# Kernel optimization log

Measured on AMD Instinct MI355X. Metric: run time of the kernel, lower is better.

Reference implementation:

```python
import jax, jax.numpy as jnp
import numpy as np

N, E, D_IN, D_OUT, R = 50000, 800000, 128, 128, 8


def setup_inputs() -> dict:
    key = jax.random.key(0)
    ks = jax.random.split(key, 6)
    x = jax.random.normal(ks[0], (N, D_IN), dtype=jnp.float32)
    W_rel = jax.random.normal(ks[1], (R, D_IN, D_OUT), dtype=jnp.float32) * (1.0 / np.sqrt(D_IN))
    W_self_w = jax.random.normal(ks[2], (D_OUT, D_IN), dtype=jnp.float32) * (1.0 / np.sqrt(D_IN))
    W_self_b = jax.random.normal(ks[3], (D_OUT,), dtype=jnp.float32) * 0.01
    edge_index = jax.random.randint(ks[4], (2, E), 0, N, dtype=jnp.int32)
    edge_type = jax.random.randint(ks[5], (E,), 0, R, dtype=jnp.int32)
    return {"x": x, "W_rel": W_rel, "W_self_w": W_self_w, "W_self_b": W_self_b,
            "edge_index": edge_index, "edge_type": edge_type}


def reference(x, W_rel, W_self_w, W_self_b, edge_index, edge_type):
    n = x.shape[0]
    # self-loop linear (nn.Linear: y = x @ W.T + b)
    out = x @ W_self_w.T + W_self_b
    src = edge_index[0]
    dst = edge_index[1]
    # Per-relation transform of all nodes: h[r, n, :] = x[n] @ W_rel[r]
    # (mathematically identical to per-edge bmm(x[src], W_rel[rel]))
    h = jnp.einsum('nd,rdo->rno', x, W_rel)  # [R, N, D_OUT]
    msg = h[edge_type, src]                   # [E, D_OUT] gather
    agg = jax.ops.segment_sum(msg, dst, num_segments=n)  # scatter-add
    deg = jax.ops.segment_sum(jnp.ones_like(dst, dtype=x.dtype), dst, num_segments=n)
    deg = jnp.maximum(deg, 1.0)[:, None]
    out = jax.nn.relu(out + agg / deg)
    # dropout p=0.0 / eval mode -> identity
    return out
```

## Files before the change

kernel.cpp:

```cpp
#include <hip/hip_runtime.h>
#include <hip/hip_bf16.h>


#define D 128
#define RNUM 8
#define KREL (RNUM * D)
#define KTOT (KREL + D)
#define ZCH 64
#define ZNB 64
#define ZSP 72

#define BSHIFT 6
#define BRANGE 64
#define BCAP   2048
#define NBKT_MAX 784
#define CSTRIDE 16

typedef short short8 __attribute__((ext_vector_type(8)));
typedef float float4v __attribute__((ext_vector_type(4)));
typedef float float2v __attribute__((ext_vector_type(2)));

static __device__ __forceinline__ unsigned int f2b(float f) {
    unsigned int u = __float_as_uint(f);
    return (u + 0x7fffu + ((u >> 16) & 1u)) >> 16;
}
static __device__ __forceinline__ float b2f_lo(unsigned int u) {
    return __uint_as_float(u << 16);
}
static __device__ __forceinline__ float b2f_hi(unsigned int u) {
    return __uint_as_float(u & 0xffff0000u);
}

static __device__ __forceinline__ void gl_lds16(const void* g, void* l) {
    __builtin_amdgcn_global_load_lds(
        (const __attribute__((address_space(1))) unsigned int*)g,
        (__attribute__((address_space(3))) unsigned int*)l, 16, 0, 0);
}

__global__ void prep_kernel(const float* __restrict__ x,
                            const float* __restrict__ W_rel,
                            const float* __restrict__ W_self,
                            unsigned short* __restrict__ xb,
                            unsigned short* __restrict__ Wcol,
                            int* __restrict__ gcur,
                            int Nn, int xb_blocks, int wc_blocks, int gz) {
    if (blockIdx.x < (unsigned)xb_blocks) {
        int t = blockIdx.x * 256 + threadIdx.x;
        int n = t >> 5;
        int c = (t & 31) * 4;
        if (n >= Nn) return;
        float4 v = *(const float4*)(x + (size_t)n * D + c);
        unsigned int p0 = f2b(v.x) | (f2b(v.y) << 16);
        unsigned int p1 = f2b(v.z) | (f2b(v.w) << 16);
        *(uint2*)(xb + (size_t)n * D + c) = make_uint2(p0, p1);
    } else if (blockIdx.x < (unsigned)(xb_blocks + wc_blocks)) {
        int idx = (blockIdx.x - xb_blocks) * 256 + threadIdx.x;
        if (idx >= KTOT * D) return;
        int c = idx >> 7;
        int k = idx & 127;
        float v = (c < KREL)
            ? W_rel[(size_t)((c >> 7) * D + k) * D + (c & 127)]
            : W_self[(size_t)(c - KREL) * D + k];
        Wcol[idx] = (unsigned short)f2b(v);
    } else {
        int idx = (blockIdx.x - xb_blocks - wc_blocks) * 256 + threadIdx.x;
        if (idx < gz) gcur[idx] = 0;
    }
}

__global__ __launch_bounds__(256) void coarse_kernel(
        const int* __restrict__ ei, const int* __restrict__ et,
        int* __restrict__ gcur, int* __restrict__ data, int E, int nbkt) {
    __shared__ int cnt[NBKT_MAX];
    int t = threadIdx.x;
    for (int i = t; i < nbkt; i += 256) cnt[i] = 0;
    __syncthreads();

    int rec[8], rb[8], rk[8];
    int e0 = blockIdx.x * 2048;
#pragma unroll
    for (int j = 0; j < 8; ++j) {
        int e = e0 + j * 256 + t;
        bool ok = e < E;
        int s = ok ? ei[e] : 0;
        int d = ok ? ei[E + e] : 0;
        int r = ok ? et[e] : 0;
        int bkt = d >> BSHIFT;
        rec[j] = s | ((d & (BRANGE - 1)) << 16) | (r << 22);
        rb[j] = ok ? bkt : -1;
        rk[j] = ok ? atomicAdd(&cnt[bkt], 1) : 0;
    }
    __syncthreads();

    for (int i = t; i < nbkt; i += 256) {
        int c = cnt[i];
        if (c) cnt[i] = i * BCAP + atomicAdd(&gcur[i * CSTRIDE], c);
    }
    __syncthreads();

#pragma unroll
    for (int j = 0; j < 8; ++j) {
        if (rb[j] >= 0) {
            int pos = cnt[rb[j]] + rk[j];
            if (pos < (rb[j] + 1) * BCAP)
                data[pos] = rec[j];
        }
    }
}

__global__ __launch_bounds__(256) void fine_kernel(
        int* __restrict__ data, const int* __restrict__ gcur,
        int* __restrict__ offsets, int* __restrict__ deg, int Nn) {
    __shared__ int recs[BCAP];
    __shared__ int hist[BRANGE * RNUM];
    int b = blockIdx.x;
    int t = threadIdx.x;
    int gbase = b * BCAP;
    int cnt = gcur[b * CSTRIDE];
    if (cnt > BCAP) cnt = BCAP;

    for (int i = t; i < BRANGE * RNUM; i += 256) hist[i] = 0;
    __syncthreads();

    for (int i = t; i < cnt; i += 256) {
        int rec = data[gbase + i];
        recs[i] = rec;
        int n = (rec >> 16) & (BRANGE - 1);
        int r = (rec >> 22) & 7;
        atomicAdd(&hist[n * RNUM + r], 1);
    }
    __syncthreads();

    if (t < BRANGE) {
        int dsum = 0;
#pragma unroll
        for (int r = 0; r < RNUM; ++r) dsum += hist[t * RNUM + r];
        int pad = (dsum + 7) & ~7;
        int x = pad;
        for (int off = 1; off < 64; off <<= 1) {
            int y = __shfl_up(x, off);
            if (t >= off) x += y;
        }
        int nb = gbase + (x - pad);
        int n0 = b * BRANGE + t;
        if (n0 < Nn) { offsets[n0] = nb; deg[n0] = dsum; }
        for (int i = dsum; i < pad; ++i)
            data[nb + i] = (int)0xF0000000u;
        int q = nb;
#pragma unroll
        for (int r = 0; r < RNUM; ++r) { int c = hist[t * RNUM + r]; hist[t * RNUM + r] = q; q += c; }
    }
    __syncthreads();

    for (int i = t; i < cnt; i += 256) {
        int rec = recs[i];
        int n = (rec >> 16) & (BRANGE - 1);
        int r = (rec >> 22) & 7;
        int pos = atomicAdd(&hist[n * RNUM + r], 1);
        data[pos] = (rec & 0xFFFF) | (r << 28);
    }
}

__global__ __launch_bounds__(256) void zgemm_kernel(
        const unsigned short* __restrict__ xb,
        const unsigned short* __restrict__ Wcol,
        unsigned short* __restrict__ Z) {
    __shared__ unsigned short Ws[ZCH * 128];
    __shared__ unsigned short Zs[ZNB * ZSP];

    const int tid  = threadIdx.x;
    const int lane = tid & 63;
    const int w    = tid >> 6;
    const int l16  = lane & 15;
    const int q    = lane >> 4;
    const int c0   = blockIdx.x * ZCH;
    const int n0   = blockIdx.y * ZNB;
    const int n    = n0 + w * 16 + l16;

    short8 xq[4];
#pragma unroll
    for (int kw = 0; kw < 4; ++kw)
        xq[kw] = *(const short8*)(xb + (size_t)n * D + kw * 32 + q * 8);

#pragma unroll
    for (int i = 0; i < 4; ++i) {
        int s = i * 256 + w * 64 + lane;
        int c = s >> 4;
        int p = (s & 15) ^ (c & 15);
        gl_lds16(Wcol + (size_t)(c0 + c) * D + p * 8,
                 &Ws[(size_t)(i * 256 + w * 64) * 8]);
    }
    __syncthreads();

    float4v acc[4] = {};
#pragma unroll
    for (int cg = 0; cg < 4; ++cg) {
#pragma unroll
        for (int kw = 0; kw < 4; ++kw) {
            short8 a = *(const short8*)(
                &Ws[(((cg * 16 + l16) << 4) + ((kw * 4 + q) ^ l16)) * 8]);
            acc[cg] = __builtin_amdgcn_mfma_f32_16x16x32_bf16(
                a, xq[kw], acc[cg], 0, 0, 0);
        }
    }

#pragma unroll
    for (int cg = 0; cg < 4; ++cg) {
        unsigned int lo = f2b(acc[cg][0]) | (f2b(acc[cg][1]) << 16);
        unsigned int hi = f2b(acc[cg][2]) | (f2b(acc[cg][3]) << 16);
        *(uint2*)(&Zs[(w * 16 + l16) * ZSP + cg * 16 + q * 4]) = make_uint2(lo, hi);
    }
    __syncthreads();

    {
        int row = tid >> 2;
        int pc  = (tid & 3) * 8;
        short8 z0 = *(const short8*)(&Zs[row * ZSP + pc]);
        short8 z1 = *(const short8*)(&Zs[row * ZSP + pc + 32]);
        unsigned short* dst = Z + (size_t)(n0 + row) * KTOT + c0;
        *(short8*)(dst + pc)      = z0;
        *(short8*)(dst + pc + 32) = z1;
    }
}

__global__ __launch_bounds__(256) void gather_kernel(
        const unsigned short* __restrict__ Z,
        const int* __restrict__ offsets,
        const int* __restrict__ deg,
        const int* __restrict__ sorted,
        const float* __restrict__ bias,
        float* __restrict__ out,
        int Nn) {
    int node = blockIdx.x * 4 + (threadIdx.x >> 6);
    if (node >= Nn) return;
    int lane = threadIdx.x & 63;
    int laneoff = lane * 2;

    int b0 = __builtin_amdgcn_readfirstlane(offsets[node]);
    int dg = __builtin_amdgcn_readfirstlane(deg[node]);
    float inv = 1.0f / fmaxf((float)dg, 1.0f);
    int bulk = dg & ~7;
    int rem  = dg & 7;

    float2v racc = {0.0f, 0.0f};

    for (int e = b0; e < b0 + bulk; e += 8) {
        int pv[8];
#pragma unroll
        for (int j = 0; j < 8; ++j)
            pv[j] = __builtin_amdgcn_readfirstlane(sorted[e + j]);
        unsigned int u[8];
#pragma unroll
        for (int j = 0; j < 8; ++j) {
            int src = pv[j] & 0xFFFF;
            int rel = (((unsigned)pv[j]) >> 28) & 7;
            u[j] = *(const unsigned int*)(Z + (size_t)src * KTOT + rel * D + laneoff);
        }
#pragma unroll
        for (int j = 0; j < 8; ++j) {
            racc.x += b2f_lo(u[j]);
            racc.y += b2f_hi(u[j]);
        }
    }
    if (rem) {
        int e = b0 + bulk;
        int pv[8];
#pragma unroll
        for (int j = 0; j < 8; ++j)
            pv[j] = __builtin_amdgcn_readfirstlane(sorted[e + j]);
        unsigned int u[8];
#pragma unroll
        for (int j = 0; j < 8; ++j) {
            int src = pv[j] & 0xFFFF;
            int rel = (((unsigned)pv[j]) >> 28) & 7;
            u[j] = *(const unsigned int*)(Z + (size_t)src * KTOT + rel * D + laneoff);
        }
#pragma unroll
        for (int j = 0; j < 8; ++j) {
            if (j < rem) {
                racc.x += b2f_lo(u[j]);
                racc.y += b2f_hi(u[j]);
            }
        }
    }

    unsigned int zs = *(const unsigned int*)(Z + (size_t)node * KTOT + KREL + laneoff);
    float bx = bias[laneoff];
    float by = bias[laneoff + 1];
    float o0 = fmaxf(b2f_lo(zs) + bx + racc.x * inv, 0.0f);
    float o1 = fmaxf(b2f_hi(zs) + by + racc.y * inv, 0.0f);
    *(float2*)(out + (size_t)node * D + laneoff) = make_float2(o0, o1);
}

extern "C" void kernel_launch(void* const* d_in, const int* in_sizes, int n_in,
                              void* d_out, int out_size, void* d_ws, size_t ws_size,
                              hipStream_t stream) {
    const float* x      = (const float*)d_in[0];
    const float* W_rel  = (const float*)d_in[1];
    const float* W_self = (const float*)d_in[2];
    const float* W_bias = (const float*)d_in[3];
    const int*   ei     = (const int*)d_in[4];
    const int*   et     = (const int*)d_in[5];

    const int Nn = in_sizes[0] / D;
    const int E  = in_sizes[4] / 2;
    const int npad = ((Nn + ZNB - 1) / ZNB) * ZNB;
    const int nbkt = (Nn + BRANGE - 1) >> BSHIFT;
    const int gz   = nbkt * CSTRIDE;

    char* p = (char*)d_ws;
    auto take = [&](size_t bytes) { char* q = p; p += (bytes + 255) & ~(size_t)255; return q; };
    unsigned short* Z    = (unsigned short*)take((size_t)npad * KTOT * sizeof(unsigned short));
    unsigned short* xb   = (unsigned short*)take((size_t)npad * D * sizeof(unsigned short));
    unsigned short* Wcol = (unsigned short*)take((size_t)KTOT * D * sizeof(unsigned short));
    int* offsets = (int*)take((size_t)Nn * sizeof(int));
    int* deg     = (int*)take((size_t)Nn * sizeof(int));
    int* gcur    = (int*)take((size_t)gz * sizeof(int));
    int* data    = (int*)take((size_t)nbkt * BCAP * sizeof(int));

    const int xb_blocks = (Nn * 32 + 255) / 256;
    const int wc_blocks = (KTOT * D + 255) / 256;
    const int gz_blocks = (gz + 255) / 256;
    prep_kernel<<<xb_blocks + wc_blocks + gz_blocks, 256, 0, stream>>>(
        x, W_rel, W_self, xb, Wcol, gcur, Nn, xb_blocks, wc_blocks, gz);
    coarse_kernel<<<(E + 2047) / 2048, 256, 0, stream>>>(ei, et, gcur, data, E, nbkt);
    fine_kernel<<<nbkt, 256, 0, stream>>>(data, gcur, offsets, deg, Nn);
    dim3 zgrid(KTOT / ZCH, npad / ZNB);
    zgemm_kernel<<<zgrid, 256, 0, stream>>>(xb, Wcol, Z);
    gather_kernel<<<(Nn + 3) / 4, 256, 0, stream>>>(Z, offsets, deg, data, W_bias,
                                                    (float*)d_out, Nn);
}
```

Baseline: 199.3 us.

## Fuse prep with coarse bucketing and zgemm with fine sort; XCD-aware strip mapping

Merges the conversion/prep kernel with the coarse edge bucketing kernel, and the Z GEMM with the fine per-node sort, into single heterogeneous launches. The counter zeroing moves to a hipMemsetAsync. The GEMM blocks are remapped so each XCD handles contiguous node strips across all 18 column chunks, which should improve L2 reuse of xb. This cuts launch count and lets the independent stages overlap on the GPU. In exchange it raises shared memory per block to the larger of the two roles and adds branch divergence between block types.

```diff
diff --git a/kernel.cpp b/kernel.cpp
--- a/kernel.cpp
+++ b/kernel.cpp
@@ -37,13 +37,16 @@
         (__attribute__((address_space(3))) unsigned int*)l, 16, 0, 0);
 }
 
-__global__ void prep_kernel(const float* __restrict__ x,
-                            const float* __restrict__ W_rel,
-                            const float* __restrict__ W_self,
-                            unsigned short* __restrict__ xb,
-                            unsigned short* __restrict__ Wcol,
-                            int* __restrict__ gcur,
-                            int Nn, int xb_blocks, int wc_blocks, int gz) {
+__global__ __launch_bounds__(256) void prep_coarse_kernel(
+        const float* __restrict__ x,
+        const float* __restrict__ W_rel,
+        const float* __restrict__ W_self,
+        const int* __restrict__ ei, const int* __restrict__ et,
+        unsigned short* __restrict__ xb,
+        unsigned short* __restrict__ Wcol,
+        int* __restrict__ gcur, int* __restrict__ data,
+        int Nn, int E, int xb_blocks, int wc_blocks, int nbkt) {
+    __shared__ int cnt[NBKT_MAX];
     if (blockIdx.x < (unsigned)xb_blocks) {
         int t = blockIdx.x * 256 + threadIdx.x;
         int n = t >> 5;
@@ -63,163 +66,167 @@
             : W_self[(size_t)(c - KREL) * D + k];
         Wcol[idx] = (unsigned short)f2b(v);
     } else {
-        int idx = (blockIdx.x - xb_blocks - wc_blocks) * 256 + threadIdx.x;
-        if (idx < gz) gcur[idx] = 0;
+        int blk = blockIdx.x - xb_blocks - wc_blocks;
+        int t = threadIdx.x;
+        for (int i = t; i < nbkt; i += 256) cnt[i] = 0;
+        __syncthreads();
+
+        int rec[8], rb[8], rk[8];
+        int e0 = blk * 2048;
+#pragma unroll
+        for (int j = 0; j < 8; ++j) {
+            int e = e0 + j * 256 + t;
+            bool ok = e < E;
+            int s = ok ? ei[e] : 0;
+            int d = ok ? ei[E + e] : 0;
+            int r = ok ? et[e] : 0;
+            int bkt = d >> BSHIFT;
+            rec[j] = s | ((d & (BRANGE - 1)) << 16) | (r << 22);
+            rb[j] = ok ? bkt : -1;
+            rk[j] = ok ? atomicAdd(&cnt[bkt], 1) : 0;
+        }
+        __syncthreads();
+
+        for (int i = t; i < nbkt; i += 256) {
+            int c = cnt[i];
+            if (c) cnt[i] = i * BCAP + atomicAdd(&gcur[i * CSTRIDE], c);
+        }
+        __syncthreads();
+
+#pragma unroll
+        for (int j = 0; j < 8; ++j) {
+            if (rb[j] >= 0) {
+                int pos = cnt[rb[j]] + rk[j];
+                if (pos < (rb[j] + 1) * BCAP)
+                    data[pos] = rec[j];
+            }
+        }
     }
 }
 
-__global__ __launch_bounds__(256) void coarse_kernel(
-        const int* __restrict__ ei, const int* __restrict__ et,
-        int* __restrict__ gcur, int* __restrict__ data, int E, int nbkt) {
-    __shared__ int cnt[NBKT_MAX];
-    int t = threadIdx.x;
-    for (int i = t; i < nbkt; i += 256) cnt[i] = 0;
-    __syncthreads();
-
-    int rec[8], rb[8], rk[8];
-    int e0 = blockIdx.x * 2048;
-#pragma unroll
-    for (int j = 0; j < 8; ++j) {
-        int e = e0 + j * 256 + t;
-        bool ok = e < E;
-        int s = ok ? ei[e] : 0;
-        int d = ok ? ei[E + e] : 0;
-        int r = ok ? et[e] : 0;
-        int bkt = d >> BSHIFT;
-        rec[j] = s | ((d & (BRANGE - 1)) << 16) | (r << 22);
-        rb[j] = ok ? bkt : -1;
-        rk[j] = ok ? atomicAdd(&cnt[bkt], 1) : 0;
-    }
-    __syncthreads();
-
-    for (int i = t; i < nbkt; i += 256) {
-        int c = cnt[i];
-        if (c) cnt[i] = i * BCAP + atomicAdd(&gcur[i * CSTRIDE], c);
-    }
-    __syncthreads();
-
-#pragma unroll
-    for (int j = 0; j < 8; ++j) {
-        if (rb[j] >= 0) {
-            int pos = cnt[rb[j]] + rk[j];
-            if (pos < (rb[j] + 1) * BCAP)
-                data[pos] = rec[j];
-        }
-    }
-}
-
-__global__ __launch_bounds__(256) void fine_kernel(
-        int* __restrict__ data, const int* __restrict__ gcur,
-        int* __restrict__ offsets, int* __restrict__ deg, int Nn) {
-    __shared__ int recs[BCAP];
-    __shared__ int hist[BRANGE * RNUM];
-    int b = blockIdx.x;
-    int t = threadIdx.x;
-    int gbase = b * BCAP;
-    int cnt = gcur[b * CSTRIDE];
-    if (cnt > BCAP) cnt = BCAP;
-
-    for (int i = t; i < BRANGE * RNUM; i += 256) hist[i] = 0;
-    __syncthreads();
-
-    for (int i = t; i < cnt; i += 256) {
-        int rec = data[gbase + i];
-        recs[i] = rec;
-        int n = (rec >> 16) & (BRANGE - 1);
-        int r = (rec >> 22) & 7;
-        atomicAdd(&hist[n * RNUM + r], 1);
-    }
-    __syncthreads();
-
-    if (t < BRANGE) {
-        int dsum = 0;
-#pragma unroll
-        for (int r = 0; r < RNUM; ++r) dsum += hist[t * RNUM + r];
-        int pad = (dsum + 7) & ~7;
-        int x = pad;
-        for (int off = 1; off < 64; off <<= 1) {
-            int y = __shfl_up(x, off);
-            if (t >= off) x += y;
-        }
-        int nb = gbase + (x - pad);
-        int n0 = b * BRANGE + t;
-        if (n0 < Nn) { offsets[n0] = nb; deg[n0] = dsum; }
-        for (int i = dsum; i < pad; ++i)
-            data[nb + i] = (int)0xF0000000u;
-        int q = nb;
-#pragma unroll
-        for (int r = 0; r < RNUM; ++r) { int c = hist[t * RNUM + r]; hist[t * RNUM + r] = q; q += c; }
-    }
-    __syncthreads();
-
-    for (int i = t; i < cnt; i += 256) {
-        int rec = recs[i];
-        int n = (rec >> 16) & (BRANGE - 1);
-        int r = (rec >> 22) & 7;
-        int pos = atomicAdd(&hist[n * RNUM + r], 1);
-        data[pos] = (rec & 0xFFFF) | (r << 28);
-    }
-}
-
-__global__ __launch_bounds__(256) void zgemm_kernel(
+__global__ __launch_bounds__(256) void zgemm_fine_kernel(
         const unsigned short* __restrict__ xb,
         const unsigned short* __restrict__ Wcol,
-        unsigned short* __restrict__ Z) {
-    __shared__ unsigned short Ws[ZCH * 128];
-    __shared__ unsigned short Zs[ZNB * ZSP];
-
-    const int tid  = threadIdx.x;
-    const int lane = tid & 63;
-    const int w    = tid >> 6;
-    const int l16  = lane & 15;
-    const int q    = lane >> 4;
-    const int c0   = blockIdx.x * ZCH;
-    const int n0   = blockIdx.y * ZNB;
-    const int n    = n0 + w * 16 + l16;
-
-    short8 xq[4];
-#pragma unroll
-    for (int kw = 0; kw < 4; ++kw)
-        xq[kw] = *(const short8*)(xb + (size_t)n * D + kw * 32 + q * 8);
-
-#pragma unroll
-    for (int i = 0; i < 4; ++i) {
-        int s = i * 256 + w * 64 + lane;
-        int c = s >> 4;
-        int p = (s & 15) ^ (c & 15);
-        gl_lds16(Wcol + (size_t)(c0 + c) * D + p * 8,
-                 &Ws[(size_t)(i * 256 + w * 64) * 8]);
-    }
-    __syncthreads();
-
-    float4v acc[4] = {};
-#pragma unroll
-    for (int cg = 0; cg < 4; ++cg) {
-#pragma unroll
-        for (int kw = 0; kw < 4; ++kw) {
-            short8 a = *(const short8*)(
-                &Ws[(((cg * 16 + l16) << 4) + ((kw * 4 + q) ^ l16)) * 8]);
-            acc[cg] = __builtin_amdgcn_mfma_f32_16x16x32_bf16(
-                a, xq[kw], acc[cg], 0, 0, 0);
-        }
-    }
-
-#pragma unroll
-    for (int cg = 0; cg < 4; ++cg) {
-        unsigned int lo = f2b(acc[cg][0]) | (f2b(acc[cg][1]) << 16);
-        unsigned int hi = f2b(acc[cg][2]) | (f2b(acc[cg][3]) << 16);
-        *(uint2*)(&Zs[(w * 16 + l16) * ZSP + cg * 16 + q * 4]) = make_uint2(lo, hi);
-    }
-    __syncthreads();
-
-    {
-        int row = tid >> 2;
-        int pc  = (tid & 3) * 8;
-        short8 z0 = *(const short8*)(&Zs[row * ZSP + pc]);
-        short8 z1 = *(const short8*)(&Zs[row * ZSP + pc + 32]);
-        unsigned short* dst = Z + (size_t)(n0 + row) * KTOT + c0;
-        *(short8*)(dst + pc)      = z0;
-        *(short8*)(dst + pc + 32) = z1;
+        unsigned short* __restrict__ Z,
+        int* __restrict__ data, const int* __restrict__ gcur,
+        int* __restrict__ offsets, int* __restrict__ deg,
+        int Nn, int nstrip, int spx, int zg) {
+    __shared__ __align__(16) char smem[25600];
+
+    if ((int)blockIdx.x < zg) {
+        unsigned short* Ws = (unsigned short*)smem;
+        unsigned short* Zs = (unsigned short*)(smem + 16384);
+
+        const int xcd = blockIdx.x & 7;
+        const int i0  = blockIdx.x >> 3;
+        const int strip = xcd * spx + i0 / 18;
+        const int chunk = i0 % 18;
+        if (strip >= nstrip) return;
+
+        const int tid  = threadIdx.x;
+        const int lane = tid & 63;
+        const int w    = tid >> 6;
+        const int l16  = lane & 15;
+        const int q    = lane >> 4;
+        const int c0   = chunk * ZCH;
+        const int n0   = strip * ZNB;
+        const int n    = n0 + w * 16 + l16;
+
+        short8 xq[4];
+#pragma unroll
+        for (int kw = 0; kw < 4; ++kw)
+            xq[kw] = *(const short8*)(xb + (size_t)n * D + kw * 32 + q * 8);
+
+#pragma unroll
+        for (int i = 0; i < 4; ++i) {
+            int s = i * 256 + w * 64 + lane;
+            int c = s >> 4;
+            int p = (s & 15) ^ (c & 15);
+            gl_lds16(Wcol + (size_t)(c0 + c) * D + p * 8,
+                     &Ws[(size_t)(i * 256 + w * 64) * 8]);
+        }
+        __syncthreads();
+
+        float4v acc[4] = {};
+#pragma unroll
+        for (int cg = 0; cg < 4; ++cg) {
+#pragma unroll
+            for (int kw = 0; kw < 4; ++kw) {
+                short8 a = *(const short8*)(
+                    &Ws[(((cg * 16 + l16) << 4) + ((kw * 4 + q) ^ l16)) * 8]);
+                acc[cg] = __builtin_amdgcn_mfma_f32_16x16x32_bf16(
+                    a, xq[kw], acc[cg], 0, 0, 0);
+            }
+        }
+
+#pragma unroll
+        for (int cg = 0; cg < 4; ++cg) {
+            unsigned int lo = f2b(acc[cg][0]) | (f2b(acc[cg][1]) << 16);
+            unsigned int hi = f2b(acc[cg][2]) | (f2b(acc[cg][3]) << 16);
+            *(uint2*)(&Zs[(w * 16 + l16) * ZSP + cg * 16 + q * 4]) = make_uint2(lo, hi);
+        }
+        __syncthreads();
+
+        {
+            int row = tid >> 2;
+            int pc  = (tid & 3) * 8;
+            short8 z0 = *(const short8*)(&Zs[row * ZSP + pc]);
+            short8 z1 = *(const short8*)(&Zs[row * ZSP + pc + 32]);
+            unsigned short* dst = Z + (size_t)(n0 + row) * KTOT + c0;
+            *(short8*)(dst + pc)      = z0;
+            *(short8*)(dst + pc + 32) = z1;
+        }
+    } else {
+        int* recs = (int*)smem;
+        int* hist = (int*)(smem + 8192);
+        int b = blockIdx.x - zg;
+        int t = threadIdx.x;
+        int gbase = b * BCAP;
+        int cnt = gcur[b * CSTRIDE];
+        if (cnt > BCAP) cnt = BCAP;
+
+        for (int i = t; i < BRANGE * RNUM; i += 256) hist[i] = 0;
+        __syncthreads();
+
+        for (int i = t; i < cnt; i += 256) {
+            int rec = data[gbase + i];
+            recs[i] = rec;
+            int n = (rec >> 16) & (BRANGE - 1);
+            int r = (rec >> 22) & 7;
+            atomicAdd(&hist[n * RNUM + r], 1);
+        }
+        __syncthreads();
+
+        if (t < BRANGE) {
+            int dsum = 0;
+#pragma unroll
+            for (int r = 0; r < RNUM; ++r) dsum += hist[t * RNUM + r];
+            int pad = (dsum + 7) & ~7;
+            int x = pad;
+            for (int off = 1; off < 64; off <<= 1) {
+                int y = __shfl_up(x, off);
+                if (t >= off) x += y;
+            }
+            int nb = gbase + (x - pad);
+            int n0 = b * BRANGE + t;
+            if (n0 < Nn) { offsets[n0] = nb; deg[n0] = dsum; }
+            for (int i = dsum; i < pad; ++i)
+                data[nb + i] = (int)0xF0000000u;
+            int q = nb;
+#pragma unroll
+            for (int r = 0; r < RNUM; ++r) {
+                int c = hist[t * RNUM + r]; hist[t * RNUM + r] = q; q += c;
+            }
+        }
+        __syncthreads();
+
+        for (int i = t; i < cnt; i += 256) {
+            int rec = recs[i];
+            int n = (rec >> 16) & (BRANGE - 1);
+            int r = (rec >> 22) & 7;
+            int pos = atomicAdd(&hist[n * RNUM + r], 1);
+            data[pos] = (rec & 0xFFFF) | (r << 28);
+        }
     }
 }
 
@@ -305,6 +312,9 @@
     const int Nn = in_sizes[0] / D;
     const int E  = in_sizes[4] / 2;
     const int npad = ((Nn + ZNB - 1) / ZNB) * ZNB;
+    const int nstrip = npad / ZNB;
+    const int spx  = (nstrip + 7) / 8;
+    const int zg   = spx * 8 * 18;
     const int nbkt = (Nn + BRANGE - 1) >> BSHIFT;
     const int gz   = nbkt * CSTRIDE;
 
@@ -320,13 +330,14 @@
 
     const int xb_blocks = (Nn * 32 + 255) / 256;
     const int wc_blocks = (KTOT * D + 255) / 256;
-    const int gz_blocks = (gz + 255) / 256;
-    prep_kernel<<<xb_blocks + wc_blocks + gz_blocks, 256, 0, stream>>>(
-        x, W_rel, W_self, xb, Wcol, gcur, Nn, xb_blocks, wc_blocks, gz);
-    coarse_kernel<<<(E + 2047) / 2048, 256, 0, stream>>>(ei, et, gcur, data, E, nbkt);
-    fine_kernel<<<nbkt, 256, 0, stream>>>(data, gcur, offsets, deg, Nn);
-    dim3 zgrid(KTOT / ZCH, npad / ZNB);
-    zgemm_kernel<<<zgrid, 256, 0, stream>>>(xb, Wcol, Z);
+    const int co_blocks = (E + 2047) / 2048;
+
+    hipMemsetAsync(gcur, 0, (size_t)gz * sizeof(int), stream);
+    prep_coarse_kernel<<<xb_blocks + wc_blocks + co_blocks, 256, 0, stream>>>(
+        x, W_rel, W_self, ei, et, xb, Wcol, gcur, data, Nn, E,
+        xb_blocks, wc_blocks, nbkt);
+    zgemm_fine_kernel<<<zg + nbkt, 256, 0, stream>>>(
+        xb, Wcol, Z, data, gcur, offsets, deg, Nn, nstrip, spx, zg);
     gather_kernel<<<(Nn + 3) / 4, 256, 0, stream>>>(Z, offsets, deg, data, W_bias,
                                                     (float*)d_out, Nn);
 }
```

Result: faster. 194.6 us (-2.3%).
